# Kernel optimization log

Measured on AMD Instinct MI355X. Metric: run time of the kernel, lower is better.

## Reference

```python
import jax, jax.numpy as jnp
import numpy as np

N = 100000
E = 1600000
C = 32          # in_channels
H = 256         # hidden_size


def setup_inputs() -> dict:
    key = jax.random.key(0)
    ks = jax.random.split(key, 16)
    s = 1.0 / np.sqrt(C)
    inp = {
        "state": jax.random.normal(ks[0], (N, C), dtype=jnp.float32),
        "edge_index": jax.random.randint(ks[1], (2, E), 0, N, dtype=jnp.int64),
        # GCNConv params (conv3 reused for layers 4 and 5, matching the source)
        "convW1": jax.random.normal(ks[2], (C, C), dtype=jnp.float32) * s,
        "convb1": jnp.zeros((C,), jnp.float32),
        "convW2": jax.random.normal(ks[3], (C, C), dtype=jnp.float32) * s,
        "convb2": jnp.zeros((C,), jnp.float32),
        "convW3": jax.random.normal(ks[4], (C, C), dtype=jnp.float32) * s,
        "convb3": jnp.zeros((C,), jnp.float32),
        "linW1": jax.random.normal(ks[5], (6 * C, H), dtype=jnp.float32) / np.sqrt(6 * C),
        "linb1": jnp.zeros((H,), jnp.float32),
        "linW2": jax.random.normal(ks[6], (H, H), dtype=jnp.float32) / np.sqrt(H),
        "linb2": jnp.zeros((H,), jnp.float32),
        "linW3": jax.random.normal(ks[7], (H, 1), dtype=jnp.float32) / np.sqrt(H),
        "linb3": jnp.zeros((1,), jnp.float32),
    }
    return inp


def _gcn(x, W, b, src, dst, norm):
    # PyG GCNConv: x' = scatter_add( norm * (xW)[src] -> dst ) + b
    xw = x @ W                                  # [N, C]
    msg = norm[:, None] * xw[src]               # [E+N, C] gather
    agg = jax.ops.segment_sum(msg, dst, num_segments=x.shape[0])
    return agg + b


def reference(state, edge_index, convW1, convb1, convW2, convb2, convW3, convb3,
              linW1, linb1, linW2, linb2, linW3, linb3):
    n = state.shape[0]
    loops = jnp.arange(n, dtype=edge_index.dtype)
    src = jnp.concatenate([edge_index[0], loops])   # add self loops
    dst = jnp.concatenate([edge_index[1], loops])
    deg = jax.ops.segment_sum(jnp.ones_like(dst, dtype=state.dtype), dst, num_segments=n)
    dinv = jnp.where(deg > 0, jax.lax.rsqrt(deg), 0.0)
    norm = dinv[src] * dinv[dst]                    # symmetric normalization

    out1 = jax.nn.relu(_gcn(state, convW1, convb1, src, dst, norm))
    out2 = jax.nn.relu(_gcn(out1, convW2, convb2, src, dst, norm))
    out3 = jax.nn.relu(_gcn(out2, convW3, convb3, src, dst, norm))
    out4 = jax.nn.relu(_gcn(out3, convW3, convb3, src, dst, norm))  # conv3 reused (as in source)
    out5 = jax.nn.relu(_gcn(out4, convW3, convb3, src, dst, norm))  # conv3 reused (as in source)

    x = jnp.concatenate([out1, out2, out3, out4, out5, state], axis=-1)  # [N, 6C]
    x = jax.nn.leaky_relu(x @ linW1 + linb1, negative_slope=0.01)
    x = jax.nn.leaky_relu(x @ linW2 + linb2, negative_slope=0.01)
    x = jax.nn.softplus(x @ linW3 + linb3)
    concentration = jnp.squeeze(x, -1)              # [N]
    # deterministic=True path
    action = concentration / (concentration.sum(axis=-1, keepdims=True) + 1e-20)
    return action
```

## Files before the change

### kernel.cpp

```cpp
#include <hip/hip_runtime.h>
#include <hip/hip_bf16.h>
#include <hip/hip_fp16.h>

#define CDIV(a,b) (((a)+(b)-1)/(b))

typedef float f32x4 __attribute__((ext_vector_type(4)));
typedef int   i32x4 __attribute__((ext_vector_type(4)));
typedef unsigned int u32x2 __attribute__((ext_vector_type(2)));

__device__ __forceinline__ void mfma16(f32x4& d, i32x4 a, i32x4 b) {
  asm("v_mfma_f32_16x16x32_bf16 %0, %1, %2, %0" : "+v"(d) : "v"(a), "v"(b));
}

__device__ __forceinline__ unsigned short bf16r(float x) {
  return __builtin_bit_cast(unsigned short, __float2bfloat16(x));
}
__device__ __forceinline__ float bf16f(unsigned short u) {
  unsigned int w_ = (unsigned int)u << 16;
  return __builtin_bit_cast(float, w_);
}


__global__ __launch_bounds__(256) void k_count(const int* __restrict__ dst,
                                               int* __restrict__ cnt, int E) {
  int e = blockIdx.x * blockDim.x + threadIdx.x;
  if (e < E) atomicAdd(&cnt[dst[e]], 1);
}

__global__ __launch_bounds__(256) void k_scan1(const int* __restrict__ cnt,
                                               int* __restrict__ rowptr,
                                               int* __restrict__ blockSums, int N) {
  __shared__ int sdata[256];
  const int t = threadIdx.x;
  const int base = blockIdx.x * 1024;
  int v[4]; int local = 0;
#pragma unroll
  for (int i = 0; i < 4; i++) {
    int idx = base + t * 4 + i;
    v[i] = (idx < N) ? cnt[idx] : 0;
    local += v[i];
  }
  sdata[t] = local;
  __syncthreads();
  for (int off = 1; off < 256; off <<= 1) {
    int x = (t >= off) ? sdata[t - off] : 0;
    __syncthreads();
    sdata[t] += x;
    __syncthreads();
  }
  if (t == 255) blockSums[blockIdx.x] = sdata[255];
  int run = sdata[t] - local;
#pragma unroll
  for (int i = 0; i < 4; i++) {
    int idx = base + t * 4 + i;
    if (idx < N) rowptr[idx] = run;
    run += v[i];
  }
}

__global__ __launch_bounds__(256) void k_scan2(int* blockSums, int NB) {
  __shared__ int sdata[256];
  int t = threadIdx.x;
  int v = (t < NB) ? blockSums[t] : 0;
  sdata[t] = v;
  __syncthreads();
  for (int off = 1; off < 256; off <<= 1) {
    int x = (t >= off) ? sdata[t - off] : 0;
    __syncthreads();
    sdata[t] += x;
    __syncthreads();
  }
  if (t < NB) blockSums[t] = sdata[t] - v;
}

__global__ __launch_bounds__(256) void k_scan3(int* __restrict__ rowptr,
                                               const int* __restrict__ blockSums,
                                               int N, int E) {
  int idx = blockIdx.x * blockDim.x + threadIdx.x;
  if (idx < N) rowptr[idx] += blockSums[idx >> 10];
  if (idx == 0) rowptr[N] = E;
}

__global__ __launch_bounds__(256) void k_fill(const int* __restrict__ src,
                                              const int* __restrict__ dst,
                                              const int* __restrict__ rowptr,
                                              int* __restrict__ cursor,
                                              int* __restrict__ colidx, int E) {
  int e = blockIdx.x * blockDim.x + threadIdx.x;
  if (e < E) {
    int d = dst[e];
    int pos = rowptr[d] + atomicAdd(&cursor[d], 1);
    colidx[pos] = src[e];
  }
}

__global__ __launch_bounds__(256) void k_dinv(const int* __restrict__ cnt,
                                              float* __restrict__ dinv, int N) {
  int i = blockIdx.x * blockDim.x + threadIdx.x;
  if (i < N) dinv[i] = rsqrtf((float)cnt[i] + 1.0f);
}

__global__ __launch_bounds__(256) void k_xw(const float* __restrict__ x,
                                            const float* __restrict__ W,
                                            const float* __restrict__ dinv,
                                            unsigned short* __restrict__ y, int N) {
  __shared__ float Ws[1024];
  int t = threadIdx.x;
#pragma unroll
  for (int i = 0; i < 4; i++) Ws[t + i * 256] = W[t + i * 256];
  __syncthreads();
  int gid = blockIdx.x * blockDim.x + t;
  int n = gid >> 4, c = (gid & 15) * 2;
  if (n < N) {
    const float4* xr4 = (const float4*)(x + (size_t)n * 32);
    float a0 = 0.f, a1 = 0.f;
#pragma unroll
    for (int k4 = 0; k4 < 8; k4++) {
      float4 xv = xr4[k4];
      int k = k4 * 4;
      a0 = fmaf(xv.x, Ws[(k + 0) * 32 + c], a0); a1 = fmaf(xv.x, Ws[(k + 0) * 32 + c + 1], a1);
      a0 = fmaf(xv.y, Ws[(k + 1) * 32 + c], a0); a1 = fmaf(xv.y, Ws[(k + 1) * 32 + c + 1], a1);
      a0 = fmaf(xv.z, Ws[(k + 2) * 32 + c], a0); a1 = fmaf(xv.z, Ws[(k + 2) * 32 + c + 1], a1);
      a0 = fmaf(xv.w, Ws[(k + 3) * 32 + c], a0); a1 = fmaf(xv.w, Ws[(k + 3) * 32 + c + 1], a1);
    }
    float dn = dinv[n];
    __half2 h = __floats2half2_rn(a0 * dn, a1 * dn);
    *(__half2*)&y[(size_t)gid * 2] = h;
  }
}

__device__ __forceinline__ void acc8(float* acc, uint4 v) {
  float2 f;
  f = __half22float2(__builtin_bit_cast(__half2, v.x)); acc[0] += f.x; acc[1] += f.y;
  f = __half22float2(__builtin_bit_cast(__half2, v.y)); acc[2] += f.x; acc[3] += f.y;
  f = __half22float2(__builtin_bit_cast(__half2, v.z)); acc[4] += f.x; acc[5] += f.y;
  f = __half22float2(__builtin_bit_cast(__half2, v.w)); acc[6] += f.x; acc[7] += f.y;
}

__global__ __launch_bounds__(256) void k_agg(const unsigned short* __restrict__ y,
                                             const int* __restrict__ rowptr,
                                             const int* __restrict__ colidx,
                                             const float* __restrict__ dinv,
                                             const float* __restrict__ b,
                                             float* __restrict__ out, int N) {
  int t = threadIdx.x;
  int q = t & 3;
  int n = blockIdx.x * 64 + (t >> 2);
  if (n >= N) return;
  const uint4* yrow = (const uint4*)y;
  float acc[8];
  {
    uint4 v = yrow[(size_t)n * 4 + q];
    float2 f;
    f = __half22float2(__builtin_bit_cast(__half2, v.x)); acc[0] = f.x; acc[1] = f.y;
    f = __half22float2(__builtin_bit_cast(__half2, v.y)); acc[2] = f.x; acc[3] = f.y;
    f = __half22float2(__builtin_bit_cast(__half2, v.z)); acc[4] = f.x; acc[5] = f.y;
    f = __half22float2(__builtin_bit_cast(__half2, v.w)); acc[6] = f.x; acc[7] = f.y;
  }
  int beg = rowptr[n], end = rowptr[n + 1];
  int j = beg;
  for (; j + 8 <= end; j += 8) {
    int s0 = colidx[j],     s1 = colidx[j + 1], s2 = colidx[j + 2], s3 = colidx[j + 3];
    int s4 = colidx[j + 4], s5 = colidx[j + 5], s6 = colidx[j + 6], s7 = colidx[j + 7];
    uint4 v0 = yrow[(size_t)s0 * 4 + q];
    uint4 v1 = yrow[(size_t)s1 * 4 + q];
    uint4 v2 = yrow[(size_t)s2 * 4 + q];
    uint4 v3 = yrow[(size_t)s3 * 4 + q];
    uint4 v4 = yrow[(size_t)s4 * 4 + q];
    uint4 v5 = yrow[(size_t)s5 * 4 + q];
    uint4 v6 = yrow[(size_t)s6 * 4 + q];
    uint4 v7 = yrow[(size_t)s7 * 4 + q];
    acc8(acc, v0); acc8(acc, v1); acc8(acc, v2); acc8(acc, v3);
    acc8(acc, v4); acc8(acc, v5); acc8(acc, v6); acc8(acc, v7);
  }
  for (; j + 4 <= end; j += 4) {
    int s0 = colidx[j], s1 = colidx[j + 1], s2 = colidx[j + 2], s3 = colidx[j + 3];
    uint4 v0 = yrow[(size_t)s0 * 4 + q];
    uint4 v1 = yrow[(size_t)s1 * 4 + q];
    uint4 v2 = yrow[(size_t)s2 * 4 + q];
    uint4 v3 = yrow[(size_t)s3 * 4 + q];
    acc8(acc, v0); acc8(acc, v1); acc8(acc, v2); acc8(acc, v3);
  }
  for (; j < end; j++) {
    uint4 v = yrow[(size_t)colidx[j] * 4 + q];
    acc8(acc, v);
  }
  float dn = dinv[n];
  int cb = q * 8;
  float4 r0, r1;
  r0.x = fmaxf(fmaf(dn, acc[0], b[cb + 0]), 0.f);
  r0.y = fmaxf(fmaf(dn, acc[1], b[cb + 1]), 0.f);
  r0.z = fmaxf(fmaf(dn, acc[2], b[cb + 2]), 0.f);
  r0.w = fmaxf(fmaf(dn, acc[3], b[cb + 3]), 0.f);
  r1.x = fmaxf(fmaf(dn, acc[4], b[cb + 4]), 0.f);
  r1.y = fmaxf(fmaf(dn, acc[5], b[cb + 5]), 0.f);
  r1.z = fmaxf(fmaf(dn, acc[6], b[cb + 6]), 0.f);
  r1.w = fmaxf(fmaf(dn, acc[7], b[cb + 7]), 0.f);
  ((float4*)out)[(size_t)n * 8 + q * 2 + 0] = r0;
  ((float4*)out)[(size_t)n * 8 + q * 2 + 1] = r1;
}

__global__ __launch_bounds__(256) void k_prepw(const float* __restrict__ W1,
                                               const float* __restrict__ W2,
                                               unsigned short* __restrict__ Wt1h,
                                               unsigned short* __restrict__ Wt1l,
                                               unsigned short* __restrict__ Wt2h,
                                               unsigned short* __restrict__ Wt2l) {
  int o = blockIdx.x * blockDim.x + threadIdx.x;
  if (o < 256 * 192) {
    int col = o / 192, k = o % 192;
    float v = W1[k * 256 + col];
    unsigned short h = bf16r(v);
    Wt1h[o] = h;
    Wt1l[o] = bf16r(v - bf16f(h));
  } else if (o < 256 * 192 + 256 * 256) {
    int o2 = o - 256 * 192;
    int col = o2 / 256, k = o2 % 256;
    float v = W2[k * 256 + col];
    unsigned short h = bf16r(v);
    Wt2h[o2] = h;
    Wt2l[o2] = bf16r(v - bf16f(h));
  }
}

__device__ __forceinline__ float softplusf(float x) {
  return fmaxf(x, 0.f) + log1pf(expf(-fabsf(x)));
}

#define XS_STRIDE 200
#define H1_STRIDE 264
#define MNODES 48

__global__ __launch_bounds__(512, 4) void k_mlp_mfma(
    const float* __restrict__ o1, const float* __restrict__ o2,
    const float* __restrict__ o3, const float* __restrict__ o4,
    const float* __restrict__ o5, const float* __restrict__ st,
    const unsigned short* __restrict__ Wt1h, const unsigned short* __restrict__ Wt1l,
    const float* __restrict__ b1,
    const unsigned short* __restrict__ Wt2h, const unsigned short* __restrict__ Wt2l,
    const float* __restrict__ b2,
    const float* __restrict__ W3, const float* __restrict__ b3,
    float* __restrict__ conc, int N) {
  __shared__ unsigned short smem[2 * MNODES * H1_STRIDE];
  __shared__ float red[8][MNODES];
  unsigned short* xsh = smem;
  unsigned short* xsl = smem + MNODES * XS_STRIDE;
  unsigned short* h1h = smem;
  unsigned short* h1l = smem + MNODES * H1_STRIDE;

  const int t = threadIdx.x;
  const int w = t >> 6;
  const int l = t & 63;
  const int l15 = l & 15, lq = l >> 4;
  const int nodeBase = blockIdx.x * MNODES;

  const float* srcs[6] = {o1, o2, o3, o4, o5, st};
  for (int i = t; i < MNODES * 96; i += 512) {
    int n = i / 96, cp = (i % 96) * 2;
    int gn = nodeBase + n;
    unsigned int pkh = 0, pkl = 0;
    if (gn < N) {
      const float* s = srcs[cp >> 5] + (size_t)gn * 32 + (cp & 31);
      float2 v = *(const float2*)s;
      unsigned short h0 = bf16r(v.x), h1_ = bf16r(v.y);
      unsigned short l0 = bf16r(v.x - bf16f(h0)), l1 = bf16r(v.y - bf16f(h1_));
      pkh = ((unsigned)h1_ << 16) | h0;
      pkl = ((unsigned)l1 << 16) | l0;
    }
    *(unsigned int*)&xsh[n * XS_STRIDE + cp] = pkh;
    *(unsigned int*)&xsl[n * XS_STRIDE + cp] = pkl;
  }
  __syncthreads();

  const int ocBase = w * 32;

  f32x4 acc[2][3];
#pragma unroll
  for (int rt = 0; rt < 2; rt++)
#pragma unroll
    for (int nt = 0; nt < 3; nt++) acc[rt][nt] = (f32x4)0.f;

  for (int kt = 0; kt < 6; kt++) {
    i32x4 ah[2], al[2];
#pragma unroll
    for (int rt = 0; rt < 2; rt++) {
      size_t aoff = (size_t)(ocBase + rt * 16 + l15) * 192 + kt * 32 + lq * 8;
      ah[rt] = *(const i32x4*)&Wt1h[aoff];
      al[rt] = *(const i32x4*)&Wt1l[aoff];
    }
#pragma unroll
    for (int nt = 0; nt < 3; nt++) {
      int boff = (nt * 16 + l15) * XS_STRIDE + kt * 32 + lq * 8;
      i32x4 bh = *(const i32x4*)&xsh[boff];
      i32x4 bl = *(const i32x4*)&xsl[boff];
#pragma unroll
      for (int rt = 0; rt < 2; rt++) mfma16(acc[rt][nt], ah[rt], bh);
#pragma unroll
      for (int rt = 0; rt < 2; rt++) mfma16(acc[rt][nt], al[rt], bh);
#pragma unroll
      for (int rt = 0; rt < 2; rt++) mfma16(acc[rt][nt], ah[rt], bl);
    }
  }
  __syncthreads();

#pragma unroll
  for (int rt = 0; rt < 2; rt++) {
    const int oc0 = ocBase + rt * 16 + lq * 4;
    float bb0 = b1[oc0], bb1 = b1[oc0 + 1], bb2 = b1[oc0 + 2], bb3 = b1[oc0 + 3];
#pragma unroll
    for (int nt = 0; nt < 3; nt++) {
      float v0 = acc[rt][nt][0] + bb0; v0 = (v0 > 0.f) ? v0 : 0.01f * v0;
      float v1 = acc[rt][nt][1] + bb1; v1 = (v1 > 0.f) ? v1 : 0.01f * v1;
      float v2 = acc[rt][nt][2] + bb2; v2 = (v2 > 0.f) ? v2 : 0.01f * v2;
      float v3 = acc[rt][nt][3] + bb3; v3 = (v3 > 0.f) ? v3 : 0.01f * v3;
      unsigned short h0 = bf16r(v0), h1_ = bf16r(v1), h2_ = bf16r(v2), h3_ = bf16r(v3);
      u32x2 pkh, pkl;
      pkh[0] = ((unsigned)h1_ << 16) | h0;
      pkh[1] = ((unsigned)h3_ << 16) | h2_;
      pkl[0] = ((unsigned)bf16r(v1 - bf16f(h1_)) << 16) | bf16r(v0 - bf16f(h0));
      pkl[1] = ((unsigned)bf16r(v3 - bf16f(h3_)) << 16) | bf16r(v2 - bf16f(h2_));
      int row = nt * 16 + l15;
      *(u32x2*)&h1h[row * H1_STRIDE + oc0] = pkh;
      *(u32x2*)&h1l[row * H1_STRIDE + oc0] = pkl;
    }
  }
  __syncthreads();

  f32x4 acc2[2][3];
#pragma unroll
  for (int rt = 0; rt < 2; rt++)
#pragma unroll
    for (int nt = 0; nt < 3; nt++) acc2[rt][nt] = (f32x4)0.f;

  for (int kt = 0; kt < 8; kt++) {
    i32x4 ah[2], al[2];
#pragma unroll
    for (int rt = 0; rt < 2; rt++) {
      size_t aoff = (size_t)(ocBase + rt * 16 + l15) * 256 + kt * 32 + lq * 8;
      ah[rt] = *(const i32x4*)&Wt2h[aoff];
      al[rt] = *(const i32x4*)&Wt2l[aoff];
    }
#pragma unroll
    for (int nt = 0; nt < 3; nt++) {
      int boff = (nt * 16 + l15) * H1_STRIDE + kt * 32 + lq * 8;
      i32x4 bh = *(const i32x4*)&h1h[boff];
      i32x4 bl = *(const i32x4*)&h1l[boff];
#pragma unroll
      for (int rt = 0; rt < 2; rt++) mfma16(acc2[rt][nt], ah[rt], bh);
#pragma unroll
      for (int rt = 0; rt < 2; rt++) mfma16(acc2[rt][nt], al[rt], bh);
#pragma unroll
      for (int rt = 0; rt < 2; rt++) mfma16(acc2[rt][nt], ah[rt], bl);
    }
  }

#pragma unroll
  for (int nt = 0; nt < 3; nt++) {
    float p = 0.f;
#pragma unroll
    for (int rt = 0; rt < 2; rt++) {
      const int oc0 = ocBase + rt * 16 + lq * 4;
#pragma unroll
      for (int j = 0; j < 4; j++) {
        float v = acc2[rt][nt][j] + b2[oc0 + j];
        v = (v > 0.f) ? v : 0.01f * v;
        p = fmaf(v, W3[oc0 + j], p);
      }
    }
    p += __shfl_xor(p, 16, 64);
    p += __shfl_xor(p, 32, 64);
    if (lq == 0) red[w][nt * 16 + l15] = p;
  }
  __syncthreads();

  if (t < MNODES) {
    int gn = nodeBase + t;
    if (gn < N) {
      float s = red[0][t] + red[1][t] + red[2][t] + red[3][t]
              + red[4][t] + red[5][t] + red[6][t] + red[7][t] + b3[0];
      conc[gn] = softplusf(s);
    }
  }
}

__global__ __launch_bounds__(256) void k_redsum(const float* __restrict__ conc,
                                                float* __restrict__ total, int N) {
  float s = 0.f;
  for (int i = blockIdx.x * blockDim.x + threadIdx.x; i < N; i += gridDim.x * blockDim.x)
    s += conc[i];
#pragma unroll
  for (int off = 32; off > 0; off >>= 1) s += __shfl_down(s, off, 64);
  __shared__ float ws_[4];
  if ((threadIdx.x & 63) == 0) ws_[threadIdx.x >> 6] = s;
  __syncthreads();
  if (threadIdx.x == 0) atomicAdd(total, ws_[0] + ws_[1] + ws_[2] + ws_[3]);
}

__global__ __launch_bounds__(256) void k_div(const float* __restrict__ conc,
                                             const float* __restrict__ total,
                                             float* __restrict__ out, int N) {
  int i = blockIdx.x * blockDim.x + threadIdx.x;
  if (i < N) out[i] = conc[i] / (total[0] + 1e-20f);
}

extern "C" void kernel_launch(void* const* d_in, const int* in_sizes, int n_in,
                              void* d_out, int out_size, void* d_ws, size_t ws_size,
                              hipStream_t stream) {
  const float* state = (const float*)d_in[0];
  const int*   ei    = (const int*)d_in[1];
  const float* cW1 = (const float*)d_in[2];
  const float* cb1 = (const float*)d_in[3];
  const float* cW2 = (const float*)d_in[4];
  const float* cb2 = (const float*)d_in[5];
  const float* cW3 = (const float*)d_in[6];
  const float* cb3 = (const float*)d_in[7];
  const float* lW1 = (const float*)d_in[8];
  const float* lb1 = (const float*)d_in[9];
  const float* lW2 = (const float*)d_in[10];
  const float* lb2 = (const float*)d_in[11];
  const float* lW3 = (const float*)d_in[12];
  const float* lb3 = (const float*)d_in[13];

  const int N = in_sizes[0] / 32;
  const int E = in_sizes[1] / 2;
  const int* srcI = ei;
  const int* dstI = ei + E;

  char* w = (char*)d_ws;
  size_t off = 0;
  auto alloc = [&](size_t bytes) -> void* {
    void* p = w + off;
    off = (off + bytes + 255) & ~(size_t)255;
    return p;
  };
  int*   cnt       = (int*)alloc((size_t)N * 4);
  int*   cursor    = (int*)alloc((size_t)N * 4);
  float* total     = (float*)alloc(256);
  size_t zbytes = off;
  int*   rowptr    = (int*)alloc(((size_t)N + 1) * 4);
  int*   blockSums = (int*)alloc(256 * 4);
  int*   colidx    = (int*)alloc((size_t)E * 4);
  float* dinv      = (float*)alloc((size_t)N * 4);
  unsigned short* ybuf = (unsigned short*)alloc((size_t)N * 32 * 2);
  float* out1      = (float*)alloc((size_t)N * 32 * 4);
  float* out2      = (float*)alloc((size_t)N * 32 * 4);
  float* out3      = (float*)alloc((size_t)N * 32 * 4);
  float* out4      = (float*)alloc((size_t)N * 32 * 4);
  float* out5      = (float*)alloc((size_t)N * 32 * 4);
  float* conc      = (float*)alloc((size_t)N * 4);
  unsigned short* Wt1h = (unsigned short*)alloc(256 * 192 * 2);
  unsigned short* Wt1l = (unsigned short*)alloc(256 * 192 * 2);
  unsigned short* Wt2h = (unsigned short*)alloc(256 * 256 * 2);
  unsigned short* Wt2l = (unsigned short*)alloc(256 * 256 * 2);

  const int TB = 256;
  hipMemsetAsync(d_ws, 0, zbytes, stream);

  k_count<<<CDIV(E, TB), TB, 0, stream>>>(dstI, cnt, E);
  int NB = CDIV(N, 1024);
  k_scan1<<<NB, TB, 0, stream>>>(cnt, rowptr, blockSums, N);
  k_scan2<<<1, TB, 0, stream>>>(blockSums, NB);
  k_scan3<<<CDIV(N, TB), TB, 0, stream>>>(rowptr, blockSums, N, E);
  k_fill<<<CDIV(E, TB), TB, 0, stream>>>(srcI, dstI, rowptr, cursor, colidx, E);
  k_dinv<<<CDIV(N, TB), TB, 0, stream>>>(cnt, dinv, N);
  k_prepw<<<CDIV(256 * 192 + 256 * 256, TB), TB, 0, stream>>>(lW1, lW2, Wt1h, Wt1l, Wt2h, Wt2l);

  struct Layer { const float* x; const float* W; const float* b; float* out; };
  Layer L[5] = {{state, cW1, cb1, out1},
                {out1,  cW2, cb2, out2},
                {out2,  cW3, cb3, out3},
                {out3,  cW3, cb3, out4},
                {out4,  cW3, cb3, out5}};
  for (int i = 0; i < 5; i++) {
    k_xw<<<CDIV(N * 16, TB), TB, 0, stream>>>(L[i].x, L[i].W, dinv, ybuf, N);
    k_agg<<<CDIV(N, 64), TB, 0, stream>>>(ybuf, rowptr, colidx, dinv, L[i].b, L[i].out, N);
  }

  k_mlp_mfma<<<CDIV(N, MNODES), 512, 0, stream>>>(out1, out2, out3, out4, out5, state,
                                                  Wt1h, Wt1l, lb1, Wt2h, Wt2l, lb2,
                                                  lW3, lb3, conc, N);
  k_redsum<<<256, TB, 0, stream>>>(conc, total, N);
  k_div<<<CDIV(N, TB), TB, 0, stream>>>(conc, total, (float*)d_out, N);
}
```

Baseline: 512.4 us.

## Unroll gather deeper, enlarge MLP node tile, drop hidden-layer low-bf16 split

```diff
diff --git a/kernel.cpp b/kernel.cpp
--- a/kernel.cpp
+++ b/kernel.cpp
@@ -159,27 +159,26 @@
   }
   int beg = rowptr[n], end = rowptr[n + 1];
   int j = beg;
+  for (; j + 16 <= end; j += 16) {
+    uint4 v[16];
+#pragma unroll
+    for (int u = 0; u < 16; u++) v[u] = yrow[(size_t)colidx[j + u] * 4 + q];
+#pragma unroll
+    for (int u = 0; u < 16; u++) acc8(acc, v[u]);
+  }
   for (; j + 8 <= end; j += 8) {
-    int s0 = colidx[j],     s1 = colidx[j + 1], s2 = colidx[j + 2], s3 = colidx[j + 3];
-    int s4 = colidx[j + 4], s5 = colidx[j + 5], s6 = colidx[j + 6], s7 = colidx[j + 7];
-    uint4 v0 = yrow[(size_t)s0 * 4 + q];
-    uint4 v1 = yrow[(size_t)s1 * 4 + q];
-    uint4 v2 = yrow[(size_t)s2 * 4 + q];
-    uint4 v3 = yrow[(size_t)s3 * 4 + q];
-    uint4 v4 = yrow[(size_t)s4 * 4 + q];
-    uint4 v5 = yrow[(size_t)s5 * 4 + q];
-    uint4 v6 = yrow[(size_t)s6 * 4 + q];
-    uint4 v7 = yrow[(size_t)s7 * 4 + q];
-    acc8(acc, v0); acc8(acc, v1); acc8(acc, v2); acc8(acc, v3);
-    acc8(acc, v4); acc8(acc, v5); acc8(acc, v6); acc8(acc, v7);
+    uint4 v[8];
+#pragma unroll
+    for (int u = 0; u < 8; u++) v[u] = yrow[(size_t)colidx[j + u] * 4 + q];
+#pragma unroll
+    for (int u = 0; u < 8; u++) acc8(acc, v[u]);
   }
   for (; j + 4 <= end; j += 4) {
-    int s0 = colidx[j], s1 = colidx[j + 1], s2 = colidx[j + 2], s3 = colidx[j + 3];
-    uint4 v0 = yrow[(size_t)s0 * 4 + q];
-    uint4 v1 = yrow[(size_t)s1 * 4 + q];
-    uint4 v2 = yrow[(size_t)s2 * 4 + q];
-    uint4 v3 = yrow[(size_t)s3 * 4 + q];
-    acc8(acc, v0); acc8(acc, v1); acc8(acc, v2); acc8(acc, v3);
+    uint4 v[4];
+#pragma unroll
+    for (int u = 0; u < 4; u++) v[u] = yrow[(size_t)colidx[j + u] * 4 + q];
+#pragma unroll
+    for (int u = 0; u < 4; u++) acc8(acc, v[u]);
   }
   for (; j < end; j++) {
     uint4 v = yrow[(size_t)colidx[j] * 4 + q];
@@ -229,7 +228,7 @@
 
 #define XS_STRIDE 200
 #define H1_STRIDE 264
-#define MNODES 48
+#define MNODES 64
 
 __global__ __launch_bounds__(512, 4) void k_mlp_mfma(
     const float* __restrict__ o1, const float* __restrict__ o2,
@@ -241,12 +240,11 @@
     const float* __restrict__ b2,
     const float* __restrict__ W3, const float* __restrict__ b3,
     float* __restrict__ conc, int N) {
-  __shared__ unsigned short smem[2 * MNODES * H1_STRIDE];
+  __shared__ unsigned short smem[2 * MNODES * XS_STRIDE];
   __shared__ float red[8][MNODES];
   unsigned short* xsh = smem;
   unsigned short* xsl = smem + MNODES * XS_STRIDE;
   unsigned short* h1h = smem;
-  unsigned short* h1l = smem + MNODES * H1_STRIDE;
 
   const int t = threadIdx.x;
   const int w = t >> 6;
@@ -274,11 +272,11 @@
 
   const int ocBase = w * 32;
 
-  f32x4 acc[2][3];
+  f32x4 acc[2][4];
 #pragma unroll
   for (int rt = 0; rt < 2; rt++)
 #pragma unroll
-    for (int nt = 0; nt < 3; nt++) acc[rt][nt] = (f32x4)0.f;
+    for (int nt = 0; nt < 4; nt++) acc[rt][nt] = (f32x4)0.f;
 
   for (int kt = 0; kt < 6; kt++) {
     i32x4 ah[2], al[2];
@@ -289,7 +287,7 @@
       al[rt] = *(const i32x4*)&Wt1l[aoff];
     }
 #pragma unroll
-    for (int nt = 0; nt < 3; nt++) {
+    for (int nt = 0; nt < 4; nt++) {
       int boff = (nt * 16 + l15) * XS_STRIDE + kt * 32 + lq * 8;
       i32x4 bh = *(const i32x4*)&xsh[boff];
       i32x4 bl = *(const i32x4*)&xsl[boff];
@@ -308,29 +306,25 @@
     const int oc0 = ocBase + rt * 16 + lq * 4;
     float bb0 = b1[oc0], bb1 = b1[oc0 + 1], bb2 = b1[oc0 + 2], bb3 = b1[oc0 + 3];
 #pragma unroll
-    for (int nt = 0; nt < 3; nt++) {
+    for (int nt = 0; nt < 4; nt++) {
       float v0 = acc[rt][nt][0] + bb0; v0 = (v0 > 0.f) ? v0 : 0.01f * v0;
       float v1 = acc[rt][nt][1] + bb1; v1 = (v1 > 0.f) ? v1 : 0.01f * v1;
       float v2 = acc[rt][nt][2] + bb2; v2 = (v2 > 0.f) ? v2 : 0.01f * v2;
       float v3 = acc[rt][nt][3] + bb3; v3 = (v3 > 0.f) ? v3 : 0.01f * v3;
-      unsigned short h0 = bf16r(v0), h1_ = bf16r(v1), h2_ = bf16r(v2), h3_ = bf16r(v3);
-      u32x2 pkh, pkl;
-      pkh[0] = ((unsigned)h1_ << 16) | h0;
-      pkh[1] = ((unsigned)h3_ << 16) | h2_;
-      pkl[0] = ((unsigned)bf16r(v1 - bf16f(h1_)) << 16) | bf16r(v0 - bf16f(h0));
-      pkl[1] = ((unsigned)bf16r(v3 - bf16f(h3_)) << 16) | bf16r(v2 - bf16f(h2_));
+      u32x2 pkh;
+      pkh[0] = ((unsigned)bf16r(v1) << 16) | bf16r(v0);
+      pkh[1] = ((unsigned)bf16r(v3) << 16) | bf16r(v2);
       int row = nt * 16 + l15;
       *(u32x2*)&h1h[row * H1_STRIDE + oc0] = pkh;
-      *(u32x2*)&h1l[row * H1_STRIDE + oc0] = pkl;
-    }
-  }
-  __syncthreads();
-
-  f32x4 acc2[2][3];
+    }
+  }
+  __syncthreads();
+
+  f32x4 acc2[2][4];
 #pragma unroll
   for (int rt = 0; rt < 2; rt++)
 #pragma unroll
-    for (int nt = 0; nt < 3; nt++) acc2[rt][nt] = (f32x4)0.f;
+    for (int nt = 0; nt < 4; nt++) acc2[rt][nt] = (f32x4)0.f;
 
   for (int kt = 0; kt < 8; kt++) {
     i32x4 ah[2], al[2];
@@ -341,21 +335,18 @@
       al[rt] = *(const i32x4*)&Wt2l[aoff];
     }
 #pragma unroll
-    for (int nt = 0; nt < 3; nt++) {
+    for (int nt = 0; nt < 4; nt++) {
       int boff = (nt * 16 + l15) * H1_STRIDE + kt * 32 + lq * 8;
       i32x4 bh = *(const i32x4*)&h1h[boff];
-      i32x4 bl = *(const i32x4*)&h1l[boff];
 #pragma unroll
       for (int rt = 0; rt < 2; rt++) mfma16(acc2[rt][nt], ah[rt], bh);
 #pragma unroll
       for (int rt = 0; rt < 2; rt++) mfma16(acc2[rt][nt], al[rt], bh);
-#pragma unroll
-      for (int rt = 0; rt < 2; rt++) mfma16(acc2[rt][nt], ah[rt], bl);
-    }
-  }
-
-#pragma unroll
-  for (int nt = 0; nt < 3; nt++) {
+    }
+  }
+
+#pragma unroll
+  for (int nt = 0; nt < 4; nt++) {
     float p = 0.f;
 #pragma unroll
     for (int rt = 0; rt < 2; rt++) {
```

New measurement: 454.3 us. 11.3% less time.
